# Kernel optimization log

Hardware: AMD Instinct MI355X
Metric: run time of the kernel (lower is better)

The kernel has to match this reference:

```python
import jax, jax.numpy as jnp
import numpy as np

B, T, C, NH = 4, 827, 1024, 16
HS = C // NH
SCALE = 1.0 / float(np.sqrt(HS))


def setup_inputs() -> dict:
    key = jax.random.key(0)
    ks = jax.random.split(key, 16)
    d = {}
    d["x"] = jax.random.normal(ks[0], (B, T, C), jnp.float32)
    d["x_kv"] = jax.random.normal(ks[1], (B, T, C), jnp.float32)
    d["h"] = jax.random.normal(ks[2], (B, NH, T, T), jnp.float32) * 0.1
    for i, name in enumerate(["f01", "f02", "f12", "b01", "b02", "b12"]):
        d[name] = jax.random.uniform(ks[3 + i], (B, 256, 256), jnp.float32)
    for i, name in enumerate(["Wq", "Wk", "Wv", "Wp"]):
        d[name] = jax.random.normal(ks[9 + i], (C, C), jnp.float32) * 0.02
    for name in ["bq", "bk", "bv", "bp"]:
        d[name] = jnp.zeros((C,), jnp.float32)
    return d


def _sm(a):
    return jax.nn.softmax(a, axis=-1)


def reference(x, x_kv, h, f01, f02, f12, b01, b02, b12,
              Wq, bq, Wk, bk, Wv, bv, Wp, bp):
    Bb, Tt, Cc = x.shape

    def heads(t):  # [B,T,C] -> [B,NH,T,HS]
        return t.reshape(Bb, Tt, NH, HS).transpose(0, 2, 1, 3)

    q = heads(x @ Wq.T + bq)
    k = heads(x_kv @ Wk.T + bk)
    v = heads(x_kv @ Wv.T + bv)

    att = jnp.einsum('bhqd,bhkd->bhqk', q, k) * SCALE + h  # adaptive bias add

    # region-specific partial softmax (frame1->frame0, frame2->frame0, frame2->frame1)
    att = att.at[:, :, 285:541, 0:256].set(_sm(att[:, :, 285:541, 0:256]))
    att = att.at[:, :, 571:827, 0:256].set(_sm(att[:, :, 571:827, 0:256]))
    att = att.at[:, :, 571:827, 286:542].set(_sm(att[:, :, 571:827, 286:542]))

    # bidirectional epipolar maps (backward maps used transposed)
    b01t = b01.transpose(0, 2, 1)
    b02t = b02.transpose(0, 2, 1)
    b12t = b12.transpose(0, 2, 1)
    m12 = (f12 * b12t >= 0.1).astype(att.dtype)  # [B,256,256]

    # bi_epi_ratio (T==827 branch), computed BEFORE the multiplicative masking
    r3 = att[:, :, 571:827, 286:542]            # [B,NH,256,256]
    att_mean = r3.mean(-1)                       # [B,NH,256]
    att_mask_mean = (r3 * m12[:, None]).sum(-1) / m12.sum(-1)[:, None]
    bi_epi_ratio = att_mask_mean.mean(1) / att_mean.mean(1)  # [B,256]

    # att_for: forward-only masking (clone); att: forward*backward masking
    att_for = att
    att_for = att_for.at[:, :, 285:541, 0:256].multiply(f01[:, None])
    att_for = att_for.at[:, :, 571:827, 0:256].multiply(f02[:, None])
    att_for = att_for.at[:, :, 571:827, 286:542].multiply(f12[:, None])
    att = att.at[:, :, 285:541, 0:256].multiply((b01t * f01)[:, None])
    att = att.at[:, :, 571:827, 0:256].multiply((b02t * f02)[:, None])
    att = att.at[:, :, 571:827, 286:542].multiply((b12t * f12)[:, None])

    causal = jnp.tril(jnp.ones((Tt, Tt), dtype=bool))
    aw = jnp.where(causal, att, -jnp.inf)
    # re-softmax of the already masked+multiplied regions (overwrites, then global softmax)
    aw = aw.at[:, :, 571:827, 0:256].set(_sm(att[:, :, 571:827, 0:256]))
    aw = aw.at[:, :, 571:827, 286:542].set(_sm(att[:, :, 571:827, 286:542]))
    aw = _sm(aw)

    y = jnp.einsum('bhqk,bhkd->bhqd', aw, v)
    y = y.transpose(0, 2, 1, 3).reshape(Bb, Tt, Cc)
    y = y @ Wp.T + bp  # resid dropout is identity (pdrop=0 / eval)
    return y, bi_epi_ratio
```

## Files before the change

### kernel.cpp

```cpp
#include <hip/hip_runtime.h>
#include <cstdint>
#include <cstddef>

#define Tn  827
#define Cn  1024
#define BTn 3308
#define TPn 832
#define YSZ 3387392

typedef unsigned short u16;
typedef unsigned short u16x4 __attribute__((ext_vector_type(4)));
typedef __bf16 bf16_t;
typedef bf16_t bf16x8 __attribute__((ext_vector_type(8)));
typedef float f32x4 __attribute__((ext_vector_type(4)));

__device__ inline u16 f32_to_bf16(float f) {
  union { float f; unsigned u; } v; v.f = f;
  unsigned u = v.u;
  u += 0x7fffu + ((u >> 16) & 1u);
  return (u16)(u >> 16);
}

__global__ __launch_bounds__(256)
void cvt_all_k(const float* __restrict__ x, const float* __restrict__ xkv,
               const float* __restrict__ wq, const float* __restrict__ wk,
               const float* __restrict__ wv, const float* __restrict__ wp,
               u16* __restrict__ xb, u16* __restrict__ xkb,
               u16* __restrict__ wqb, u16* __restrict__ wkb,
               u16* __restrict__ wvb, u16* __restrict__ wpb)
{
  const long NX = 846848;
  const long NW = 262144;
  long qidx = (long)blockIdx.x * 256 + threadIdx.x;
  const float* s; u16* d; long base;
  if (qidx < NX)            { s = x;   d = xb;  base = qidx; }
  else if (qidx < 2 * NX)   { s = xkv; d = xkb; base = qidx - NX; }
  else {
    long w = qidx - 2 * NX;
    int wi = (int)(w / NW);
    base = w - (long)wi * NW;
    if      (wi == 0) { s = wq; d = wqb; }
    else if (wi == 1) { s = wk; d = wkb; }
    else if (wi == 2) { s = wv; d = wvb; }
    else if (wi == 3) { s = wp; d = wpb; }
    else return;
  }
  const float4 v = *(const float4*)(s + base * 4);
  u16x4 o;
  o.x = f32_to_bf16(v.x); o.y = f32_to_bf16(v.y);
  o.z = f32_to_bf16(v.z); o.w = f32_to_bf16(v.w);
  *(u16x4*)(d + base * 4) = o;
}

template<int BM, int BN, int MODE>
__global__ __launch_bounds__(256)
void gemm_k(const u16* __restrict__ Aall, const u16* __restrict__ Ball,
            const float* __restrict__ bias, float* __restrict__ Cf,
            u16* __restrict__ Cb, int M, int N, int K, int lda, int ldb, int ldc)
{
  static_assert(BM == 128, "BM fixed at 128");
  constexpr int TM = BM / 32;
  constexpr int TN = BN / 32;

  const int tid  = threadIdx.x;
  const int lane = tid & 63;
  const int wave = tid >> 6;
  const int wm = wave >> 1, wn = wave & 1;
  const int m0 = blockIdx.x * BM;
  const int n0 = blockIdx.y * BN;

  __shared__ u16 As[BM * 32];
  __shared__ u16 Bs[BN * 32];

  f32x4 acc[TM][TN];
  const f32x4 zero4 = {0.f, 0.f, 0.f, 0.f};
  #pragma unroll
  for (int i = 0; i < TM; ++i)
    #pragma unroll
    for (int j = 0; j < TN; ++j)
      acc[i][j] = zero4;

  const int nk = K >> 5;

  for (int kt = 0; kt < nk; ++kt) {
    const int k0 = kt << 5;
    __syncthreads();
    #pragma unroll
    for (int it = 0; it < BM / 64; ++it) {
      const int cbase = it * 256 + wave * 64;
      const int c  = cbase + lane;
      const int r  = c >> 2;
      const int ko = (c & 3) << 3;
      if (m0 + r < M)
        __builtin_amdgcn_global_load_lds(
            (__attribute__((address_space(1))) void*)(Aall + (size_t)(m0 + r) * lda + k0 + ko),
            (__attribute__((address_space(3))) void*)(As + cbase * 8),
            16, 0, 0);
    }
    #pragma unroll
    for (int it = 0; it < BN / 64; ++it) {
      const int cbase = it * 256 + wave * 64;
      const int c  = cbase + lane;
      const int r  = c >> 2;
      const int ko = (c & 3) << 3;
      if (n0 + r < N)
        __builtin_amdgcn_global_load_lds(
            (__attribute__((address_space(1))) void*)(Ball + (size_t)(n0 + r) * ldb + k0 + ko),
            (__attribute__((address_space(3))) void*)(Bs + cbase * 8),
            16, 0, 0);
    }
    __syncthreads();

    bf16x8 af[TM], bfr[TN];
    #pragma unroll
    for (int i = 0; i < TM; ++i) {
      const int r = wm * 64 + i * 16 + (lane & 15);
      af[i] = *(const bf16x8*)(As + r * 32 + ((lane >> 4) << 3));
    }
    #pragma unroll
    for (int j = 0; j < TN; ++j) {
      const int r = wn * (TN * 16) + j * 16 + (lane & 15);
      bfr[j] = *(const bf16x8*)(Bs + r * 32 + ((lane >> 4) << 3));
    }
    #pragma unroll
    for (int i = 0; i < TM; ++i)
      #pragma unroll
      for (int j = 0; j < TN; ++j)
        acc[i][j] = __builtin_amdgcn_mfma_f32_16x16x32_bf16(af[i], bfr[j], acc[i][j], 0, 0, 0);
  }

  const int cq = lane >> 4, cl = lane & 15;
  #pragma unroll
  for (int i = 0; i < TM; ++i) {
    #pragma unroll
    for (int j = 0; j < TN; ++j) {
      const int rb  = m0 + wm * 64 + i * 16 + cq * 4;
      const int col = n0 + wn * (TN * 16) + j * 16 + cl;
      #pragma unroll
      for (int r = 0; r < 4; ++r) {
        const int row = rb + r;
        const float v = acc[i][j][r];
        if constexpr (MODE == 0) {
          if (row < M) Cb[(size_t)row * ldc + col] = f32_to_bf16(v + bias[col]);
        } else {
          if (row < M) Cf[(size_t)row * ldc + col] = v + bias[col];
        }
      }
    }
  }
}

__global__ __launch_bounds__(256)
void vtrans_k(const u16* __restrict__ V, u16* __restrict__ Vt)
{
  const int z = blockIdx.y;
  const int b = z >> 4, hh = z & 15;
  const int k0 = blockIdx.x * 64;
  const int tid = threadIdx.x;
  __shared__ u16 tile[64 * 65];
  #pragma unroll
  for (int rep = 0; rep < 16; ++rep) {
    const int idx = rep * 256 + tid;
    const int kl = idx >> 6, n = idx & 63;
    const int k = k0 + kl;
    u16 val = 0;
    if (k < Tn) val = V[((size_t)(b * Tn + k)) * Cn + hh * 64 + n];
    tile[n * 65 + kl] = val;
  }
  __syncthreads();
  #pragma unroll
  for (int rep = 0; rep < 16; ++rep) {
    const int idx = rep * 256 + tid;
    const int n = idx >> 6, kl = idx & 63;
    const int k = k0 + kl;
    if (k < TPn) Vt[((size_t)z * 64 + n) * TPn + k] = tile[n * 65 + kl];
  }
}

__global__ __launch_bounds__(256)
void btrans_k(const float* __restrict__ b01, const float* __restrict__ b02,
              const float* __restrict__ b12, float* __restrict__ bT)
{
  const int mb = blockIdx.z;
  const int rg = mb >> 2, bb = mb & 3;
  const float* src = (rg == 0 ? b01 : rg == 1 ? b02 : b12) + (size_t)bb * 65536;
  float* dst = bT + (size_t)mb * 65536;
  const int i0 = blockIdx.x * 64, j0 = blockIdx.y * 64;
  __shared__ float tile[64 * 65];
  const int tid = threadIdx.x;
  #pragma unroll
  for (int rep = 0; rep < 16; ++rep) {
    const int idx = rep * 256 + tid;
    const int jj = idx >> 6, ii = idx & 63;
    tile[ii * 65 + jj] = src[(size_t)(j0 + jj) * 256 + i0 + ii];
  }
  __syncthreads();
  #pragma unroll
  for (int rep = 0; rep < 16; ++rep) {
    const int idx = rep * 256 + tid;
    const int ii = idx >> 6, jj = idx & 63;
    dst[(size_t)(i0 + ii) * 256 + j0 + jj] = tile[ii * 65 + jj];
  }
}

__global__ __launch_bounds__(256)
void sreg_k(const u16* __restrict__ Qb, const u16* __restrict__ Kb,
            const float* __restrict__ hsrc, float* __restrict__ Sreg)
{
  const int zr = blockIdx.z;
  const int rg = zr % 3;
  const int z  = zr / 3;
  const int b = z >> 4, hh = z & 15;
  const int qoff = (rg == 0) ? 285 : 571;
  const int koff = (rg == 2) ? 286 : 0;
  const int m0 = blockIdx.x * 64;
  const int n0 = blockIdx.y * 64;

  const int tid = threadIdx.x;
  const int lane = tid & 63, wave = tid >> 6;
  const int quad = lane >> 4, cl = lane & 15;
  const int wm = wave >> 1, wn = wave & 1;

  __shared__ u16 As[2048], Bs[2048];

  const u16* Ab = Qb + ((size_t)(b * Tn + qoff + m0)) * Cn + hh * 64;
  const u16* Bb = Kb + ((size_t)(b * Tn + koff + n0)) * Cn + hh * 64;

  f32x4 acc[2][2];
  const f32x4 zero4 = {0.f, 0.f, 0.f, 0.f};
  acc[0][0] = zero4; acc[0][1] = zero4; acc[1][0] = zero4; acc[1][1] = zero4;

  #pragma unroll
  for (int kt = 0; kt < 2; ++kt) {
    const int k0 = kt * 32;
    __syncthreads();
    const int r = tid >> 2, ko = (tid & 3) << 3;
    __builtin_amdgcn_global_load_lds(
        (__attribute__((address_space(1))) void*)(Ab + (size_t)r * Cn + k0 + ko),
        (__attribute__((address_space(3))) void*)(&As[wave * 512]), 16, 0, 0);
    __builtin_amdgcn_global_load_lds(
        (__attribute__((address_space(1))) void*)(Bb + (size_t)r * Cn + k0 + ko),
        (__attribute__((address_space(3))) void*)(&Bs[wave * 512]), 16, 0, 0);
    __syncthreads();
    bf16x8 af[2], bfr[2];
    #pragma unroll
    for (int i = 0; i < 2; ++i)
      af[i] = *(const bf16x8*)(&As[(wm * 32 + i * 16 + cl) * 32 + quad * 8]);
    #pragma unroll
    for (int j = 0; j < 2; ++j)
      bfr[j] = *(const bf16x8*)(&Bs[(wn * 32 + j * 16 + cl) * 32 + quad * 8]);
    #pragma unroll
    for (int i = 0; i < 2; ++i)
      #pragma unroll
      for (int j = 0; j < 2; ++j)
        acc[i][j] = __builtin_amdgcn_mfma_f32_16x16x32_bf16(af[i], bfr[j], acc[i][j], 0, 0, 0);
  }

  float hvv[2][2][4];
  const size_t hb0 = (size_t)z * Tn * Tn;
  #pragma unroll
  for (int i = 0; i < 2; ++i)
    #pragma unroll
    for (int j = 0; j < 2; ++j)
      #pragma unroll
      for (int r = 0; r < 4; ++r) {
        const int row = m0 + wm * 32 + i * 16 + quad * 4 + r;
        const int col = n0 + wn * 32 + j * 16 + cl;
        hvv[i][j][r] = hsrc[hb0 + (size_t)(qoff + row) * Tn + koff + col];
      }
  float* outb = Sreg + ((size_t)zr << 16);
  #pragma unroll
  for (int i = 0; i < 2; ++i)
    #pragma unroll
    for (int j = 0; j < 2; ++j)
      #pragma unroll
      for (int r = 0; r < 4; ++r) {
        const int row = m0 + wm * 32 + i * 16 + quad * 4 + r;
        const int col = n0 + wn * 32 + j * 16 + cl;
        outb[(size_t)row * 256 + col] = acc[i][j][r] * 0.125f + hvv[i][j][r];
      }
}

__global__ __launch_bounds__(256)
void regional_k(float* __restrict__ Sreg, const float* __restrict__ f01,
                const float* __restrict__ f02, const float* __restrict__ f12,
                const float* __restrict__ bT,
                float* __restrict__ mmOut, float* __restrict__ amOut)
{
  const int tid  = threadIdx.x;
  const int lane = tid & 63;
  const int wrow = tid >> 6;
  const int row_id = blockIdx.x * 4 + wrow;
  const int region = row_id >> 14;
  const int rr = row_id & 16383;
  const int b  = rr >> 12;
  const int hh = (rr >> 8) & 15;
  const int i  = rr & 255;
  float* rp = Sreg + ((size_t)(((b * 16 + hh) * 3) + region) << 16) + (size_t)i * 256;

  const float* fp = (region == 0) ? f01 : (region == 1) ? f02 : f12;
  const float* bp = bT + ((size_t)(region * 4 + b) << 16);

  float v[4], fv[4], bv[4];
  #pragma unroll
  for (int t = 0; t < 4; ++t) {
    const int j = lane + 64 * t;
    v[t]  = rp[j];
    fv[t] = fp[((size_t)b * 256 + i) * 256 + j];
    bv[t] = bp[(size_t)i * 256 + j];
  }
  float mx = fmaxf(fmaxf(v[0], v[1]), fmaxf(v[2], v[3]));
  for (int m = 32; m > 0; m >>= 1) mx = fmaxf(mx, __shfl_xor(mx, m));
  float e[4], s = 0.f;
  #pragma unroll
  for (int t = 0; t < 4; ++t) { e[t] = __expf(v[t] - mx); s += e[t]; }
  for (int m = 32; m > 0; m >>= 1) s += __shfl_xor(s, m);
  const float inv = 1.f / s;
  float sm[4];
  #pragma unroll
  for (int t = 0; t < 4; ++t) sm[t] = e[t] * inv;

  if (region == 2) {
    float msum = 0.f, mcnt = 0.f, asum = 0.f;
    #pragma unroll
    for (int t = 0; t < 4; ++t) {
      const float mk = (fv[t] * bv[t] >= 0.1f) ? 1.f : 0.f;
      msum += sm[t] * mk; mcnt += mk; asum += sm[t];
    }
    for (int m = 32; m > 0; m >>= 1) {
      msum += __shfl_xor(msum, m);
      mcnt += __shfl_xor(mcnt, m);
      asum += __shfl_xor(asum, m);
    }
    if (lane == 0) {
      const int idx = (b * 16 + hh) * 256 + i;
      mmOut[idx] = msum / mcnt;
      amOut[idx] = asum * (1.f / 256.f);
    }
  }

  float mult[4];
  #pragma unroll
  for (int t = 0; t < 4; ++t) mult[t] = sm[t] * fv[t] * bv[t];

  if (region == 0) {
    #pragma unroll
    for (int t = 0; t < 4; ++t) rp[lane + 64 * t] = mult[t];
  } else {
    float mx2 = fmaxf(fmaxf(mult[0], mult[1]), fmaxf(mult[2], mult[3]));
    for (int m = 32; m > 0; m >>= 1) mx2 = fmaxf(mx2, __shfl_xor(mx2, m));
    float e2[4], s2 = 0.f;
    #pragma unroll
    for (int t = 0; t < 4; ++t) { e2[t] = __expf(mult[t] - mx2); s2 += e2[t]; }
    for (int m = 32; m > 0; m >>= 1) s2 += __shfl_xor(s2, m);
    const float inv2 = 1.f / s2;
    #pragma unroll
    for (int t = 0; t < 4; ++t) rp[lane + 64 * t] = e2[t] * inv2;
  }
}

__global__ __launch_bounds__(256)
void flash_k(const u16* __restrict__ Qb, const u16* __restrict__ Kb,
             const u16* __restrict__ Vt, const float* __restrict__ hsrc,
             const float* __restrict__ Sreg, u16* __restrict__ ya)
{
  const int bid = blockIdx.x;
  const int zlow = bid & 7;
  const int t = bid >> 3;
  const int qt = t % 13;
  const int zhigh = t / 13;
  const int z = zhigh * 8 + zlow;
  const int b = z >> 4, hh = z & 15;
  const int q0 = qt * 64;

  const int tid = threadIdx.x;
  const int lane = tid & 63;
  const int wave = tid >> 6;
  const int quad = lane >> 4;
  const int cl = lane & 15;

  __shared__ u16 Qs[2][2048];
  __shared__ u16 Ks[2][2048];
  __shared__ u16 Vs[2][2048];
  __shared__ u16 Ps[4][2][512];

  {
    const u16* src = Qb + ((size_t)(b * Tn + q0)) * Cn + hh * 64;
    const int r = tid >> 2;
    const int ko = (tid & 3) << 3;
    #pragma unroll
    for (int p = 0; p < 2; ++p)
      __builtin_amdgcn_global_load_lds(
          (__attribute__((address_space(1))) void*)(src + (size_t)r * Cn + p * 32 + ko),
          (__attribute__((address_space(3))) void*)(&Qs[p][wave * 512]), 16, 0, 0);
  }
  __syncthreads();

  bf16x8 qa[2];
  #pragma unroll
  for (int p = 0; p < 2; ++p)
    qa[p] = *(const bf16x8*)(&Qs[p][(wave * 16 + cl) * 32 + quad * 8]);

  f32x4 Oa[4];
  const f32x4 zero4 = {0.f, 0.f, 0.f, 0.f};
  Oa[0] = zero4; Oa[1] = zero4; Oa[2] = zero4; Oa[3] = zero4;
  float mrow[4] = {-3.0e38f, -3.0e38f, -3.0e38f, -3.0e38f};
  float lrow[4] = {0.f, 0.f, 0.f, 0.f};

  const size_t hbase = (size_t)z * Tn * Tn;
  const int qrow_base = q0 + wave * 16 + quad * 4;

  for (int kt = 0; kt <= qt; ++kt) {
    const int k0 = kt * 64;
    __syncthreads();
    {
      const u16* ksrc = Kb + ((size_t)(b * Tn + k0)) * Cn + hh * 64;
      const u16* vsrc = Vt + ((size_t)(z * 64)) * TPn + k0;
      const int r = tid >> 2;
      const int ko = (tid & 3) << 3;
      #pragma unroll
      for (int p = 0; p < 2; ++p) {
        __builtin_amdgcn_global_load_lds(
            (__attribute__((address_space(1))) void*)(ksrc + (size_t)r * Cn + p * 32 + ko),
            (__attribute__((address_space(3))) void*)(&Ks[p][wave * 512]), 16, 0, 0);
        __builtin_amdgcn_global_load_lds(
            (__attribute__((address_space(1))) void*)(vsrc + (size_t)r * TPn + p * 32 + ko),
            (__attribute__((address_space(3))) void*)(&Vs[p][wave * 512]), 16, 0, 0);
      }
    }
    float hv[4][4];
    unsigned rmask = 0;
    #pragma unroll
    for (int j = 0; j < 4; ++j) {
      const int kk = k0 + j * 16 + cl;
      #pragma unroll
      for (int r = 0; r < 4; ++r) {
        const int qq = qrow_base + r;
        const float* p = hsrc + hbase + (size_t)qq * Tn + kk;
        bool isreg = false;
        if (kk < 542) {
          if (qq >= 571 && qq < Tn) {
            if (kk < 256) {
              p = Sreg + (((size_t)(z * 3 + 1)) << 16) + (size_t)(qq - 571) * 256 + kk;
              isreg = true;
            } else if (kk >= 286) {
              p = Sreg + (((size_t)(z * 3 + 2)) << 16) + (size_t)(qq - 571) * 256 + (kk - 286);
              isreg = true;
            }
          } else if (qq >= 285 && qq < 541 && kk < 256) {
            p = Sreg + (((size_t)(z * 3 + 0)) << 16) + (size_t)(qq - 285) * 256 + kk;
            isreg = true;
          }
        }
        const bool valid = (kk <= qq) && (qq < Tn);
        hv[j][r] = valid ? *p : 0.f;
        if (isreg) rmask |= 1u << (j * 4 + r);
      }
    }
    __syncthreads();

    f32x4 sa[4];
    sa[0] = zero4; sa[1] = zero4; sa[2] = zero4; sa[3] = zero4;
    #pragma unroll
    for (int p = 0; p < 2; ++p) {
      #pragma unroll
      for (int n = 0; n < 4; ++n) {
        const bf16x8 kb = *(const bf16x8*)(&Ks[p][(n * 16 + cl) * 32 + quad * 8]);
        sa[n] = __builtin_amdgcn_mfma_f32_16x16x32_bf16(qa[p], kb, sa[n], 0, 0, 0);
      }
    }

    #pragma unroll
    for (int r = 0; r < 4; ++r) {
      const int qq = qrow_base + r;
      float sv[4];
      #pragma unroll
      for (int j = 0; j < 4; ++j) {
        const int kk = k0 + j * 16 + cl;
        const float vv = ((rmask >> (j * 4 + r)) & 1)
                             ? hv[j][r]
                             : sa[j][r] * 0.125f + hv[j][r];
        sv[j] = (kk <= qq && qq < Tn) ? vv : -3.0e38f;
      }
      float mx = fmaxf(fmaxf(sv[0], sv[1]), fmaxf(sv[2], sv[3]));
      mx = fmaxf(mx, __shfl_xor(mx, 1));
      mx = fmaxf(mx, __shfl_xor(mx, 2));
      mx = fmaxf(mx, __shfl_xor(mx, 4));
      mx = fmaxf(mx, __shfl_xor(mx, 8));
      const float mnew = fmaxf(mrow[r], mx);
      const float alpha = __expf(mrow[r] - mnew);
      mrow[r] = mnew;
      float ps[4], psum = 0.f;
      #pragma unroll
      for (int j = 0; j < 4; ++j) { ps[j] = __expf(sv[j] - mnew); psum += ps[j]; }
      psum += __shfl_xor(psum, 1);
      psum += __shfl_xor(psum, 2);
      psum += __shfl_xor(psum, 4);
      psum += __shfl_xor(psum, 8);
      lrow[r] = lrow[r] * alpha + psum;
      #pragma unroll
      for (int n = 0; n < 4; ++n) Oa[n][r] *= alpha;
      #pragma unroll
      for (int j = 0; j < 4; ++j)
        Ps[wave][j >> 1][(quad * 4 + r) * 32 + (j & 1) * 16 + cl] = f32_to_bf16(ps[j]);
    }

    #pragma unroll
    for (int p = 0; p < 2; ++p) {
      const bf16x8 pa = *(const bf16x8*)(&Ps[wave][p][cl * 32 + quad * 8]);
      #pragma unroll
      for (int n = 0; n < 4; ++n) {
        const bf16x8 vb = *(const bf16x8*)(&Vs[p][(n * 16 + cl) * 32 + quad * 8]);
        Oa[n] = __builtin_amdgcn_mfma_f32_16x16x32_bf16(pa, vb, Oa[n], 0, 0, 0);
      }
    }
  }

  #pragma unroll
  for (int r = 0; r < 4; ++r) {
    const int qq = qrow_base + r;
    if (qq >= Tn) continue;
    const float inv = 1.f / lrow[r];
    u16* op = ya + ((size_t)(b * Tn + qq)) * Cn + hh * 64;
    #pragma unroll
    for (int n = 0; n < 4; ++n)
      op[n * 16 + cl] = f32_to_bf16(Oa[n][r] * inv);
  }
}

__global__ __launch_bounds__(256)
void ratio_k(const float* __restrict__ mm, const float* __restrict__ am,
             float* __restrict__ out)
{
  const int idx = blockIdx.x * 256 + threadIdx.x;
  const int b = idx >> 8, i = idx & 255;
  float smm = 0.f, sam = 0.f;
  #pragma unroll
  for (int hh = 0; hh < 16; ++hh) {
    smm += mm[(b * 16 + hh) * 256 + i];
    sam += am[(b * 16 + hh) * 256 + i];
  }
  out[idx] = smm / sam;
}

extern "C" void kernel_launch(void* const* d_in, const int* in_sizes, int n_in,
                              void* d_out, int out_size, void* d_ws, size_t ws_size,
                              hipStream_t stream)
{
  (void)in_sizes; (void)n_in; (void)out_size;

  const float* x   = (const float*)d_in[0];
  const float* xkv = (const float*)d_in[1];
  const float* hb  = (const float*)d_in[2];
  const float* f01 = (const float*)d_in[3];
  const float* f02 = (const float*)d_in[4];
  const float* f12 = (const float*)d_in[5];
  const float* b01 = (const float*)d_in[6];
  const float* b02 = (const float*)d_in[7];
  const float* b12 = (const float*)d_in[8];
  const float* Wq  = (const float*)d_in[9];
  const float* Wk  = (const float*)d_in[10];
  const float* Wv  = (const float*)d_in[11];
  const float* Wp  = (const float*)d_in[12];
  const float* bq  = (const float*)d_in[13];
  const float* bk  = (const float*)d_in[14];
  const float* bv  = (const float*)d_in[15];
  const float* bp  = (const float*)d_in[16];
  float* out = (float*)d_out;

  char* ws = (char*)d_ws;
  u16* xb   = (u16*)(ws + 0);
  u16* xkb  = (u16*)(ws + 6774784);
  u16* wqb  = (u16*)(ws + 13549568);
  u16* wkb  = (u16*)(ws + 15646720);
  u16* wvb  = (u16*)(ws + 17743872);
  u16* wpb  = (u16*)(ws + 19841024);
  u16* Qb   = (u16*)(ws + 21938176);
  u16* Kb   = (u16*)(ws + 28712960);
  u16* Vb   = (u16*)(ws + 35487744);
  u16* Vt   = (u16*)(ws + 42262528);
  u16* ya   = (u16*)(ws + 49078272);
  float* Sreg = (float*)(ws + 55853056);
  float* bT = (float*)(ws + 106184704);
  float* mm = (float*)(ws + 109330432);
  float* am = (float*)(ws + 109395968);
  const size_t need = 109461504;
  if (ws_size < need) return;

  cvt_all_k<<<dim3(10712), 256, 0, stream>>>(x, xkv, Wq, Wk, Wv, Wp,
                                             xb, xkb, wqb, wkb, wvb, wpb);
  btrans_k<<<dim3(4, 4, 12), 256, 0, stream>>>(b01, b02, b12, bT);
  gemm_k<128,64,0><<<dim3(26,16,1),256,0,stream>>>(xb,  wqb, bq, nullptr, Qb, BTn, Cn, Cn, Cn, Cn, Cn);
  gemm_k<128,64,0><<<dim3(26,16,1),256,0,stream>>>(xkb, wkb, bk, nullptr, Kb, BTn, Cn, Cn, Cn, Cn, Cn);
  gemm_k<128,64,0><<<dim3(26,16,1),256,0,stream>>>(xkb, wvb, bv, nullptr, Vb, BTn, Cn, Cn, Cn, Cn, Cn);
  vtrans_k<<<dim3(13,64),256,0,stream>>>(Vb, Vt);
  sreg_k<<<dim3(4,4,192),256,0,stream>>>(Qb, Kb, hb, Sreg);
  regional_k<<<dim3(12288),256,0,stream>>>(Sreg, f01, f02, f12, bT, mm, am);
  flash_k<<<dim3(832),256,0,stream>>>(Qb, Kb, Vt, hb, Sreg, ya);
  gemm_k<128,64,3><<<dim3(26,16,1),256,0,stream>>>(ya, wpb, bp, out, nullptr, BTn, Cn, Cn, Cn, Cn, Cn);
  ratio_k<<<dim3(4),256,0,stream>>>(mm, am, out + YSZ);
}
```

Measured before the change: 472.3 us.

## Fuse QKV projections with V transpose and merge regional score/softmax kernels

Replaces the three separate Q/K/V projection GEMMs with one batched launch on larger 128x128 tiles. The V projection writes straight into the transposed per-head layout, so the separate transpose kernel and the Vb buffer go away; the padding columns of Vt are now zeroed inside the conversion kernel. Region score computation, softmax, masking, ratio statistics and the second softmax are fused into one kernel that keeps full 256-wide rows in registers, removing a round trip of the region scores through global memory. The costs are fewer GEMM blocks per launch, scattered 2-byte stores for the transposed V, and higher register pressure in the fused region kernel.

```diff
diff --git a/kernel.cpp b/kernel.cpp
--- a/kernel.cpp
+++ b/kernel.cpp
@@ -27,7 +27,8 @@
                const float* __restrict__ wv, const float* __restrict__ wp,
                u16* __restrict__ xb, u16* __restrict__ xkb,
                u16* __restrict__ wqb, u16* __restrict__ wkb,
-               u16* __restrict__ wvb, u16* __restrict__ wpb)
+               u16* __restrict__ wvb, u16* __restrict__ wpb,
+               u16* __restrict__ Vt)
 {
   const long NX = 846848;
   const long NW = 262144;
@@ -38,18 +39,136 @@
   else {
     long w = qidx - 2 * NX;
     int wi = (int)(w / NW);
+    if (wi >= 4) {
+      long p = w - 4 * NW;
+      if (p < 20480) {
+        int row = (int)(p / 5);
+        int col = 827 + (int)(p - (long)row * 5);
+        Vt[(size_t)row * TPn + col] = 0;
+      }
+      return;
+    }
     base = w - (long)wi * NW;
     if      (wi == 0) { s = wq; d = wqb; }
     else if (wi == 1) { s = wk; d = wkb; }
     else if (wi == 2) { s = wv; d = wvb; }
-    else if (wi == 3) { s = wp; d = wpb; }
-    else return;
+    else              { s = wp; d = wpb; }
   }
   const float4 v = *(const float4*)(s + base * 4);
   u16x4 o;
   o.x = f32_to_bf16(v.x); o.y = f32_to_bf16(v.y);
   o.z = f32_to_bf16(v.z); o.w = f32_to_bf16(v.w);
   *(u16x4*)(d + base * 4) = o;
+}
+
+__global__ __launch_bounds__(256)
+void gemm_qkv_k(const u16* __restrict__ xb, const u16* __restrict__ xkb,
+                const u16* __restrict__ wqb, const u16* __restrict__ wkb,
+                const u16* __restrict__ wvb,
+                const float* __restrict__ bq, const float* __restrict__ bk,
+                const float* __restrict__ bv,
+                u16* __restrict__ Qb, u16* __restrict__ Kb, u16* __restrict__ Vt)
+{
+  const int zz = blockIdx.z;
+  const u16* A  = (zz == 0) ? xb : xkb;
+  const u16* Bw = (zz == 0) ? wqb : (zz == 1) ? wkb : wvb;
+  const float* bias = (zz == 0) ? bq : (zz == 1) ? bk : bv;
+
+  const int tid  = threadIdx.x;
+  const int lane = tid & 63;
+  const int wave = tid >> 6;
+  const int wm = wave >> 1, wn = wave & 1;
+  const int m0 = blockIdx.x * 128;
+  const int n0 = blockIdx.y * 128;
+
+  __shared__ u16 As[128 * 32];
+  __shared__ u16 Bs[128 * 32];
+
+  f32x4 acc[4][4];
+  const f32x4 zero4 = {0.f, 0.f, 0.f, 0.f};
+  #pragma unroll
+  for (int i = 0; i < 4; ++i)
+    #pragma unroll
+    for (int j = 0; j < 4; ++j)
+      acc[i][j] = zero4;
+
+  for (int kt = 0; kt < 32; ++kt) {
+    const int k0 = kt << 5;
+    __syncthreads();
+    #pragma unroll
+    for (int it = 0; it < 2; ++it) {
+      const int cbase = it * 256 + wave * 64;
+      const int c  = cbase + lane;
+      const int r  = c >> 2;
+      const int ko = (c & 3) << 3;
+      if (m0 + r < BTn)
+        __builtin_amdgcn_global_load_lds(
+            (__attribute__((address_space(1))) void*)(A + (size_t)(m0 + r) * Cn + k0 + ko),
+            (__attribute__((address_space(3))) void*)(As + cbase * 8),
+            16, 0, 0);
+      __builtin_amdgcn_global_load_lds(
+          (__attribute__((address_space(1))) void*)(Bw + (size_t)(n0 + r) * Cn + k0 + ko),
+          (__attribute__((address_space(3))) void*)(Bs + cbase * 8),
+          16, 0, 0);
+    }
+    __syncthreads();
+
+    bf16x8 af[4], bfr[4];
+    #pragma unroll
+    for (int i = 0; i < 4; ++i) {
+      const int r = wm * 64 + i * 16 + (lane & 15);
+      af[i] = *(const bf16x8*)(As + r * 32 + ((lane >> 4) << 3));
+    }
+    #pragma unroll
+    for (int j = 0; j < 4; ++j) {
+      const int r = wn * 64 + j * 16 + (lane & 15);
+      bfr[j] = *(const bf16x8*)(Bs + r * 32 + ((lane >> 4) << 3));
+    }
+    #pragma unroll
+    for (int i = 0; i < 4; ++i)
+      #pragma unroll
+      for (int j = 0; j < 4; ++j)
+        acc[i][j] = __builtin_amdgcn_mfma_f32_16x16x32_bf16(af[i], bfr[j], acc[i][j], 0, 0, 0);
+  }
+
+  const int cq = lane >> 4, cl = lane & 15;
+  if (zz < 2) {
+    u16* D = (zz == 0) ? Qb : Kb;
+    #pragma unroll
+    for (int i = 0; i < 4; ++i) {
+      #pragma unroll
+      for (int j = 0; j < 4; ++j) {
+        const int rb  = m0 + wm * 64 + i * 16 + cq * 4;
+        const int col = n0 + wn * 64 + j * 16 + cl;
+        const float bc = bias[col];
+        #pragma unroll
+        for (int r = 0; r < 4; ++r) {
+          const int row = rb + r;
+          if (row < BTn) D[(size_t)row * Cn + col] = f32_to_bf16(acc[i][j][r] + bc);
+        }
+      }
+    }
+  } else {
+    #pragma unroll
+    for (int j = 0; j < 4; ++j) {
+      const int col = n0 + wn * 64 + j * 16 + cl;
+      const int hh = col >> 6, dd = col & 63;
+      const float bc = bias[col];
+      #pragma unroll
+      for (int i = 0; i < 4; ++i) {
+        const int rb = m0 + wm * 64 + i * 16 + cq * 4;
+        #pragma unroll
+        for (int r = 0; r < 4; ++r) {
+          const int row = rb + r;
+          if (row < BTn) {
+            const int bb = row / Tn;
+            const int t  = row - bb * Tn;
+            Vt[((size_t)((bb * 16 + hh) * 64 + dd)) * TPn + t] = f32_to_bf16(acc[i][j][r] + bc);
+          }
+        }
+      }
+    }
+  }
 }
 
 template<int BM, int BN, int MODE>
@@ -147,33 +266,6 @@
         }
       }
     }
-  }
-}
-
-__global__ __launch_bounds__(256)
-void vtrans_k(const u16* __restrict__ V, u16* __restrict__ Vt)
-{
-  const int z = blockIdx.y;
-  const int b = z >> 4, hh = z & 15;
-  const int k0 = blockIdx.x * 64;
-  const int tid = threadIdx.x;
-  __shared__ u16 tile[64 * 65];
-  #pragma unroll
-  for (int rep = 0; rep < 16; ++rep) {
-    const int idx = rep * 256 + tid;
-    const int kl = idx >> 6, n = idx & 63;
-    const int k = k0 + kl;
-    u16 val = 0;
-    if (k < Tn) val = V[((size_t)(b * Tn + k)) * Cn + hh * 64 + n];
-    tile[n * 65 + kl] = val;
-  }
-  __syncthreads();
-  #pragma unroll
-  for (int rep = 0; rep < 16; ++rep) {
-    const int idx = rep * 256 + tid;
-    const int n = idx >> 6, kl = idx & 63;
-    const int k = k0 + kl;
-    if (k < TPn) Vt[((size_t)z * 64 + n) * TPn + k] = tile[n * 65 + kl];
   }
 }
 
@@ -204,159 +296,200 @@
 }
 
 __global__ __launch_bounds__(256)
-void sreg_k(const u16* __restrict__ Qb, const u16* __restrict__ Kb,
-            const float* __restrict__ hsrc, float* __restrict__ Sreg)
+void regfused_k(const u16* __restrict__ Qb, const u16* __restrict__ Kb,
+                const float* __restrict__ hsrc,
+                const float* __restrict__ f01, const float* __restrict__ f02,
+                const float* __restrict__ f12, const float* __restrict__ bT,
+                float* __restrict__ Sreg, float* __restrict__ mmOut,
+                float* __restrict__ amOut)
 {
-  const int zr = blockIdx.z;
+  const int zr = blockIdx.y;
   const int rg = zr % 3;
   const int z  = zr / 3;
   const int b = z >> 4, hh = z & 15;
   const int qoff = (rg == 0) ? 285 : 571;
   const int koff = (rg == 2) ? 286 : 0;
   const int m0 = blockIdx.x * 64;
-  const int n0 = blockIdx.y * 64;
-
-  const int tid = threadIdx.x;
-  const int lane = tid & 63, wave = tid >> 6;
+
+  const int tid = threadIdx.x, lane = tid & 63, wave = tid >> 6;
   const int quad = lane >> 4, cl = lane & 15;
-  const int wm = wave >> 1, wn = wave & 1;
-
-  __shared__ u16 As[2048], Bs[2048];
-
-  const u16* Ab = Qb + ((size_t)(b * Tn + qoff + m0)) * Cn + hh * 64;
-  const u16* Bb = Kb + ((size_t)(b * Tn + koff + n0)) * Cn + hh * 64;
-
-  f32x4 acc[2][2];
+
+  __shared__ u16 Qs[2 * 2048];
+  __shared__ u16 Ks[2 * 8192];
+
+  const u16* qsrc = Qb + ((size_t)(b * Tn + qoff + m0)) * Cn + hh * 64;
+  const u16* ksrc = Kb + ((size_t)(b * Tn + koff)) * Cn + hh * 64;
+  {
+    const int r  = tid >> 2;
+    const int ko = (tid & 3) << 3;
+    #pragma unroll
+    for (int p = 0; p < 2; ++p) {
+      __builtin_amdgcn_global_load_lds(
+          (__attribute__((address_space(1))) void*)(qsrc + (size_t)r * Cn + p * 32 + ko),
+          (__attribute__((address_space(3))) void*)(&Qs[p * 2048 + wave * 512]), 16, 0, 0);
+      #pragma unroll
+      for (int it = 0; it < 4; ++it) {
+        const int c  = it * 256 + tid;
+        const int rr = c >> 2;
+        const int kko = (c & 3) << 3;
+        __builtin_amdgcn_global_load_lds(
+            (__attribute__((address_space(1))) void*)(ksrc + (size_t)rr * Cn + p * 32 + kko),
+            (__attribute__((address_space(3))) void*)(&Ks[p * 8192 + it * 2048 + wave * 512]), 16, 0, 0);
+      }
+    }
+  }
+  __syncthreads();
+
+  bf16x8 qa[2];
+  #pragma unroll
+  for (int p = 0; p < 2; ++p)
+    qa[p] = *(const bf16x8*)(&Qs[p * 2048 + (wave * 16 + cl) * 32 + quad * 8]);
+
+  f32x4 acc[16];
   const f32x4 zero4 = {0.f, 0.f, 0.f, 0.f};
-  acc[0][0] = zero4; acc[0][1] = zero4; acc[1][0] = zero4; acc[1][1] = zero4;
-
-  #pragma unroll
-  for (int kt = 0; kt < 2; ++kt) {
-    const int k0 = kt * 32;
-    __syncthreads();
-    const int r = tid >> 2, ko = (tid & 3) << 3;
-    __builtin_amdgcn_global_load_lds(
-        (__attribute__((address_space(1))) void*)(Ab + (size_t)r * Cn + k0 + ko),
-        (__attribute__((address_space(3))) void*)(&As[wave * 512]), 16, 0, 0);
-    __builtin_amdgcn_global_load_lds(
-        (__attribute__((address_space(1))) void*)(Bb + (size_t)r * Cn + k0 + ko),
-        (__attribute__((address_space(3))) void*)(&Bs[wave * 512]), 16, 0, 0);
-    __syncthreads();
-    bf16x8 af[2], bfr[2];
-    #pragma unroll
-    for (int i = 0; i < 2; ++i)
-      af[i] = *(const bf16x8*)(&As[(wm * 32 + i * 16 + cl) * 32 + quad * 8]);
-    #pragma unroll
-    for (int j = 0; j < 2; ++j)
-      bfr[j] = *(const bf16x8*)(&Bs[(wn * 32 + j * 16 + cl) * 32 + quad * 8]);
-    #pragma unroll
-    for (int i = 0; i < 2; ++i)
-      #pragma unroll
-      for (int j = 0; j < 2; ++j)
-        acc[i][j] = __builtin_amdgcn_mfma_f32_16x16x32_bf16(af[i], bfr[j], acc[i][j], 0, 0, 0);
-  }
-
-  float hvv[2][2][4];
-  const size_t hb0 = (size_t)z * Tn * Tn;
-  #pragma unroll
-  for (int i = 0; i < 2; ++i)
-    #pragma unroll
-    for (int j = 0; j < 2; ++j)
+  #pragma unroll
+  for (int n = 0; n < 16; ++n) acc[n] = zero4;
+
+  #pragma unroll
+  for (int p = 0; p < 2; ++p)
+    #pragma unroll
+    for (int n = 0; n < 16; ++n) {
+      const bf16x8 kb = *(const bf16x8*)(&Ks[p * 8192 + (n * 16 + cl) * 32 + quad * 8]);
+      acc[n] = __builtin_amdgcn_mfma_f32_16x16x32_bf16(qa[p], kb, acc[n], 0, 0, 0);
+    }
+
+  const int i0 = m0 + wave * 16 + quad * 4;
+  const float* hp = hsrc + (size_t)z * Tn * Tn + (size_t)(qoff + i0) * Tn + koff + cl;
+  #pragma unroll
+  for (int nb = 0; nb < 4; ++nb) {
+    float hv[4][4];
+    #pragma unroll
+    for (int n2 = 0; n2 < 4; ++n2)
+      #pragma unroll
+      for (int r = 0; r < 4; ++r)
+        hv[n2][r] = hp[(size_t)r * Tn + (nb * 4 + n2) * 16];
+    #pragma unroll
+    for (int n2 = 0; n2 < 4; ++n2)
+      #pragma unroll
+      for (int r = 0; r < 4; ++r)
+        acc[nb * 4 + n2][r] = acc[nb * 4 + n2][r] * 0.125f + hv[n2][r];
+  }
+
+  float red[4];
+  #pragma unroll
+  for (int r = 0; r < 4; ++r) {
+    float m = acc[0][r];
+    #pragma unroll
+    for (int n = 1; n < 16; ++n) m = fmaxf(m, acc[n][r]);
+    m = fmaxf(m, __shfl_xor(m, 1));
+    m = fmaxf(m, __shfl_xor(m, 2));
+    m = fmaxf(m, __shfl_xor(m, 4));
+    m = fmaxf(m, __shfl_xor(m, 8));
+    red[r] = m;
+  }
+  #pragma unroll
+  for (int n = 0; n < 16; ++n)
+    #pragma unroll
+    for (int r = 0; r < 4; ++r)
+      acc[n][r] = __expf(acc[n][r] - red[r]);
+  #pragma unroll
+  for (int r = 0; r < 4; ++r) {
+    float s = 0.f;
+    #pragma unroll
+    for (int n = 0; n < 16; ++n) s += acc[n][r];
+    s += __shfl_xor(s, 1); s += __shfl_xor(s, 2);
+    s += __shfl_xor(s, 4); s += __shfl_xor(s, 8);
+    const float inv = 1.f / s;
+    #pragma unroll
+    for (int n = 0; n < 16; ++n) acc[n][r] *= inv;
+  }
+
+  const float* fp  = (rg == 0) ? f01 : (rg == 1) ? f02 : f12;
+  const float* fpb = fp + ((size_t)b * 256 + i0) * 256 + cl;
+  const float* bpb = bT + (((size_t)(rg * 4 + b)) << 16) + (size_t)i0 * 256 + cl;
+  float msum[4] = {0.f, 0.f, 0.f, 0.f};
+  float mcnt[4] = {0.f, 0.f, 0.f, 0.f};
+  float asum[4] = {0.f, 0.f, 0.f, 0.f};
+  #pragma unroll
+  for (int nb = 0; nb < 4; ++nb) {
+    float fv[4][4], bv[4][4];
+    #pragma unroll
+    for (int n2 = 0; n2 < 4; ++n2)
       #pragma unroll
       for (int r = 0; r < 4; ++r) {
-        const int row = m0 + wm * 32 + i * 16 + quad * 4 + r;
-        const int col = n0 + wn * 32 + j * 16 + cl;
-        hvv[i][j][r] = hsrc[hb0 + (size_t)(qoff + row) * Tn + koff + col];
-      }
-  float* outb = Sreg + ((size_t)zr << 16);
-  #pragma unroll
-  for (int i = 0; i < 2; ++i)
-    #pragma unroll
-    for (int j = 0; j < 2; ++j)
+        fv[n2][r] = fpb[(size_t)r * 256 + (nb * 4 + n2) * 16];
+        bv[n2][r] = bpb[(size_t)r * 256 + (nb * 4 + n2) * 16];
+      }
+    #pragma unroll
+    for (int n2 = 0; n2 < 4; ++n2)
       #pragma unroll
       for (int r = 0; r < 4; ++r) {
-        const int row = m0 + wm * 32 + i * 16 + quad * 4 + r;
-        const int col = n0 + wn * 32 + j * 16 + cl;
-        outb[(size_t)row * 256 + col] = acc[i][j][r] * 0.125f + hvv[i][j][r];
-      }
-}
-
-__global__ __launch_bounds__(256)
-void regional_k(float* __restrict__ Sreg, const float* __restrict__ f01,
-                const float* __restrict__ f02, const float* __restrict__ f12,
-                const float* __restrict__ bT,
-                float* __restrict__ mmOut, float* __restrict__ amOut)
-{
-  const int tid  = threadIdx.x;
-  const int lane = tid & 63;
-  const int wrow = tid >> 6;
-  const int row_id = blockIdx.x * 4 + wrow;
-  const int region = row_id >> 14;
-  const int rr = row_id & 16383;
-  const int b  = rr >> 12;
-  const int hh = (rr >> 8) & 15;
-  const int i  = rr & 255;
-  float* rp = Sreg + ((size_t)(((b * 16 + hh) * 3) + region) << 16) + (size_t)i * 256;
-
-  const float* fp = (region == 0) ? f01 : (region == 1) ? f02 : f12;
-  const float* bp = bT + ((size_t)(region * 4 + b) << 16);
-
-  float v[4], fv[4], bv[4];
-  #pragma unroll
-  for (int t = 0; t < 4; ++t) {
-    const int j = lane + 64 * t;
-    v[t]  = rp[j];
-    fv[t] = fp[((size_t)b * 256 + i) * 256 + j];
-    bv[t] = bp[(size_t)i * 256 + j];
-  }
-  float mx = fmaxf(fmaxf(v[0], v[1]), fmaxf(v[2], v[3]));
-  for (int m = 32; m > 0; m >>= 1) mx = fmaxf(mx, __shfl_xor(mx, m));
-  float e[4], s = 0.f;
-  #pragma unroll
-  for (int t = 0; t < 4; ++t) { e[t] = __expf(v[t] - mx); s += e[t]; }
-  for (int m = 32; m > 0; m >>= 1) s += __shfl_xor(s, m);
-  const float inv = 1.f / s;
-  float sm[4];
-  #pragma unroll
-  for (int t = 0; t < 4; ++t) sm[t] = e[t] * inv;
-
-  if (region == 2) {
-    float msum = 0.f, mcnt = 0.f, asum = 0.f;
-    #pragma unroll
-    for (int t = 0; t < 4; ++t) {
-      const float mk = (fv[t] * bv[t] >= 0.1f) ? 1.f : 0.f;
-      msum += sm[t] * mk; mcnt += mk; asum += sm[t];
-    }
-    for (int m = 32; m > 0; m >>= 1) {
-      msum += __shfl_xor(msum, m);
-      mcnt += __shfl_xor(mcnt, m);
-      asum += __shfl_xor(asum, m);
-    }
-    if (lane == 0) {
-      const int idx = (b * 16 + hh) * 256 + i;
-      mmOut[idx] = msum / mcnt;
-      amOut[idx] = asum * (1.f / 256.f);
-    }
-  }
-
-  float mult[4];
-  #pragma unroll
-  for (int t = 0; t < 4; ++t) mult[t] = sm[t] * fv[t] * bv[t];
-
-  if (region == 0) {
-    #pragma unroll
-    for (int t = 0; t < 4; ++t) rp[lane + 64 * t] = mult[t];
-  } else {
-    float mx2 = fmaxf(fmaxf(mult[0], mult[1]), fmaxf(mult[2], mult[3]));
-    for (int m = 32; m > 0; m >>= 1) mx2 = fmaxf(mx2, __shfl_xor(mx2, m));
-    float e2[4], s2 = 0.f;
-    #pragma unroll
-    for (int t = 0; t < 4; ++t) { e2[t] = __expf(mult[t] - mx2); s2 += e2[t]; }
-    for (int m = 32; m > 0; m >>= 1) s2 += __shfl_xor(s2, m);
-    const float inv2 = 1.f / s2;
-    #pragma unroll
-    for (int t = 0; t < 4; ++t) rp[lane + 64 * t] = e2[t] * inv2;
-  }
+        const int n = nb * 4 + n2;
+        const float prod = fv[n2][r] * bv[n2][r];
+        if (rg == 2) {
+          const float mk = (prod >= 0.1f) ? 1.f : 0.f;
+          msum[r] += acc[n][r] * mk;
+          mcnt[r] += mk;
+          asum[r] += acc[n][r];
+        }
+        acc[n][r] *= prod;
+      }
+  }
+  if (rg == 2) {
+    #pragma unroll
+    for (int r = 0; r < 4; ++r) {
+      msum[r] += __shfl_xor(msum[r], 1); msum[r] += __shfl_xor(msum[r], 2);
+      msum[r] += __shfl_xor(msum[r], 4); msum[r] += __shfl_xor(msum[r], 8);
+      mcnt[r] += __shfl_xor(mcnt[r], 1); mcnt[r] += __shfl_xor(mcnt[r], 2);
+      mcnt[r] += __shfl_xor(mcnt[r], 4); mcnt[r] += __shfl_xor(mcnt[r], 8);
+      asum[r] += __shfl_xor(asum[r], 1); asum[r] += __shfl_xor(asum[r], 2);
+      asum[r] += __shfl_xor(asum[r], 4); asum[r] += __shfl_xor(asum[r], 8);
+    }
+    if (cl == 0) {
+      #pragma unroll
+      for (int r = 0; r < 4; ++r) {
+        const int idx = ((b * 16 + hh) << 8) + i0 + r;
+        mmOut[idx] = msum[r] / mcnt[r];
+        amOut[idx] = asum[r] * (1.f / 256.f);
+      }
+    }
+  }
+
+  if (rg != 0) {
+    #pragma unroll
+    for (int r = 0; r < 4; ++r) {
+      float m = acc[0][r];
+      #pragma unroll
+      for (int n = 1; n < 16; ++n) m = fmaxf(m, acc[n][r]);
+      m = fmaxf(m, __shfl_xor(m, 1));
+      m = fmaxf(m, __shfl_xor(m, 2));
+      m = fmaxf(m, __shfl_xor(m, 4));
+      m = fmaxf(m, __shfl_xor(m, 8));
+      red[r] = m;
+    }
+    #pragma unroll
+    for (int n = 0; n < 16; ++n)
+      #pragma unroll
+      for (int r = 0; r < 4; ++r)
+        acc[n][r] = __expf(acc[n][r] - red[r]);
+    #pragma unroll
+    for (int r = 0; r < 4; ++r) {
+      float s = 0.f;
+      #pragma unroll
+      for (int n = 0; n < 16; ++n) s += acc[n][r];
+      s += __shfl_xor(s, 1); s += __shfl_xor(s, 2);
+      s += __shfl_xor(s, 4); s += __shfl_xor(s, 8);
+      const float inv = 1.f / s;
+      #pragma unroll
+      for (int n = 0; n < 16; ++n) acc[n][r] *= inv;
+    }
+  }
+  float* outp = Sreg + (((size_t)zr) << 16) + (size_t)i0 * 256 + cl;
+  #pragma unroll
+  for (int n = 0; n < 16; ++n)
+    #pragma unroll
+    for (int r = 0; r < 4; ++r)
+      outp[(size_t)r * 256 + n * 16] = acc[n][r];
 }
 
 __global__ __launch_bounds__(256)
@@ -577,7 +710,6 @@
   u16* wpb  = (u16*)(ws + 19841024);
   u16* Qb   = (u16*)(ws + 21938176);
   u16* Kb   = (u16*)(ws + 28712960);
-  u16* Vb   = (u16*)(ws + 35487744);
   u16* Vt   = (u16*)(ws + 42262528);
   u16* ya   = (u16*)(ws + 49078272);
   float* Sreg = (float*)(ws + 55853056);
@@ -587,16 +719,15 @@
   const size_t need = 109461504;
   if (ws_size < need) return;
 
-  cvt_all_k<<<dim3(10712), 256, 0, stream>>>(x, xkv, Wq, Wk, Wv, Wp,
-                                             xb, xkb, wqb, wkb, wvb, wpb);
+  cvt_all_k<<<dim3(10792), 256, 0, stream>>>(x, xkv, Wq, Wk, Wv, Wp,
+                                             xb, xkb, wqb, wkb, wvb, wpb, Vt);
   btrans_k<<<dim3(4, 4, 12), 256, 0, stream>>>(b01, b02, b12, bT);
-  gemm_k<128,64,0><<<dim3(26,16,1),256,0,stream>>>(xb,  wqb, bq, nullptr, Qb, BTn, Cn, Cn, Cn, Cn, Cn);
-  gemm_k<128,64,0><<<dim3(26,16,1),256,0,stream>>>(xkb, wkb, bk, nullptr, Kb, BTn, Cn, Cn, Cn, Cn, Cn);
-  gemm_k<128,64,0><<<dim3(26,16,1),256,0,stream>>>(xkb, wvb, bv, nullptr, Vb, BTn, Cn, Cn, Cn, Cn, Cn);
-  vtrans_k<<<dim3(13,64),256,0,stream>>>(Vb, Vt);
-  sreg_k<<<dim3(4,4,192),256,0,stream>>>(Qb, Kb, hb, Sreg);
-  regional_k<<<dim3(12288),256,0,stream>>>(Sreg, f01, f02, f12, bT, mm, am);
-  flash_k<<<dim3(832),256,0,stream>>>(Qb, Kb, Vt, hb, Sreg, ya);
-  gemm_k<128,64,3><<<dim3(26,16,1),256,0,stream>>>(ya, wpb, bp, out, nullptr, BTn, Cn, Cn, Cn, Cn, Cn);
-  ratio_k<<<dim3(4),256,0,stream>>>(mm, am, out + YSZ);
-}
+  gemm_qkv_k<<<dim3(26, 8, 3), 256, 0, stream>>>(xb, xkb, wqb, wkb, wvb,
+                                                 bq, bk, bv, Qb, Kb, Vt);
+  regfused_k<<<dim3(4, 192), 256, 0, stream>>>(Qb, Kb, hb, f01, f02, f12, bT,
+                                               Sreg, mm, am);
+  ratio_k<<<dim3(4), 256, 0, stream>>>(mm, am, out + YSZ);
+  flash_k<<<dim3(832), 256, 0, stream>>>(Qb, Kb, Vt, hb, Sreg, ya);
+  gemm_k<128, 64, 3><<<dim3(26, 16, 1), 256, 0, stream>>>(ya, wpb, bp, out, nullptr,
+                                                          BTn, Cn, Cn, Cn, Cn, Cn);
+}
```

Result: faster. 421.0 us (-10.9%).
